# Performance work log

Measured on AMD Instinct MI355X. Metric: run time of the kernel, lower is better.

Reference implementation:

```python
import jax, jax.numpy as jnp
import numpy as np

NTIPS = 128   # taxa
NSITES = 1024 # unique site patterns
BS = 32       # batch of trees


def _make_pairs(ntips, bs, seed=0):
    """Valid postorder child/parent triples for random caterpillar trees.

    Mirrors Parsimony._score's child_parent_pairs: [ntips-1, bs, 3], where the
    last step's torch parent=-1 is rewritten to the last state slot 2*ntips-2.
    """
    rng = np.random.default_rng(seed)
    N = 2 * ntips - 1
    pairs = np.zeros((ntips - 1, bs, 3), dtype=np.int32)
    for b in range(bs):
        leaves = rng.permutation(ntips)
        pairs[0, b] = [leaves[0], leaves[1], ntips]
        for i in range(1, ntips - 3):
            pairs[i, b] = [ntips + i - 1, leaves[i + 1], ntips + i]
        root = 2 * ntips - 3
        pairs[ntips - 3, b] = [2 * ntips - 4, leaves[ntips - 2], root]
        pairs[ntips - 2, b] = [root, leaves[ntips - 1], N - 1]
    return pairs


def setup_inputs() -> dict:
    key = jax.random.key(0)
    k1, k2 = jax.random.split(key)
    # one-hot nucleotide states over 5 symbols (A,G,C,T,-)
    nuc = jax.random.randint(k1, (NTIPS, NSITES), 0, 4)
    L = jax.nn.one_hot(nuc, 5, dtype=jnp.int32).transpose(0, 2, 1)  # [ntips,5,S]
    site_counts = jax.random.randint(k2, (NSITES,), 1, 100).astype(jnp.int32)
    pairs = jnp.asarray(_make_pairs(NTIPS, BS))  # [ntips-1, bs, 3]
    return {"L": L, "site_counts": site_counts, "pairs": pairs}


def reference(L, site_counts, pairs):
    ntips, _, S = L.shape
    steps, bs, _ = pairs.shape
    N = 2 * ntips - 1
    base = jnp.concatenate(
        [L, jnp.zeros((N - ntips, 5, S), dtype=L.dtype)], axis=0)  # [N,5,S]
    state0 = jnp.tile(base[None], (bs, 1, 1, 1))   # [bs,N,5,S]
    score0 = jnp.zeros((bs, S), jnp.int32)
    barange = jnp.arange(bs)

    def step(carry, pair):
        state, score = carry
        child, parent = pair[:, :2], pair[:, 2]            # [bs,2], [bs]
        cs = state[barange[:, None], child]                # gather -> [bs,2,5,S]
        inter = cs[:, 0] * cs[:, 1]                        # [bs,5,S]
        union = ((cs[:, 0] + cs[:, 1]) > 0).astype(L.dtype)
        empty = inter.sum(axis=1, keepdims=True) == 0      # [bs,1,S]
        nxt = jnp.where(empty, union, inter)               # Fitch rule
        state = state.at[barange, parent].set(nxt)         # scatter
        score = score + empty[:, 0].astype(jnp.int32)
        return (state, score), None

    (_, score), _ = jax.lax.scan(step, (state0, score0), pairs)
    return jnp.sum(score * site_counts[None, :], axis=-1)  # [bs]
```

## Files before the change

kernel.cpp:

```cpp
#include <hip/hip_runtime.h>
#include <stdint.h>

#define NTIPS 128
#define NSITES 1024
#define BS 32
#define STEPS 127
#define NINTERNAL 127

__global__ __launch_bounds__(1024) void fitch_kernel(
    const int* __restrict__ L,
    const int* __restrict__ site_counts,
    const int* __restrict__ pairs,
    uint8_t* __restrict__ ws,
    int* __restrict__ out)
{
    __shared__ int spairs[STEPS * 3];
    __shared__ int wsum[16];
    __shared__ int allvalid;

    const int tid  = threadIdx.x;
    const int b    = blockIdx.x;
    const int site = tid;

    if (tid == 0) allvalid = 1;
    if (tid < STEPS * 3) {
        int s = tid / 3, j = tid - s * 3;
        spairs[tid] = pairs[s * (BS * 3) + b * 3 + j];
    }
    __syncthreads();

    if (tid < STEPS) {
        int c0 = spairs[3 * tid], c1 = spairs[3 * tid + 1], p = spairs[3 * tid + 2];
        bool v = (c1 >= 0) && (c1 < NTIPS) && (p >= NTIPS) &&
                 (tid == 0 ? (c0 >= 0 && c0 < NTIPS)
                           : (c0 == spairs[3 * (tid - 1) + 2]));
        if (!v) allvalid = 0;
    }
    __syncthreads();

    const int* Lp = L + site;
    int score = 0;

    #define LEAFMASK(q) ((q)[0] | ((q)[NSITES] << 1) | ((q)[2 * NSITES] << 2) | \
                         ((q)[3 * NSITES] << 3) | ((q)[4 * NSITES] << 4))

    if (allvalid) {
        int c00 = __builtin_amdgcn_readfirstlane(spairs[0]);
        const int* q0 = Lp + c00 * 5 * NSITES;
        int cur = LEAFMASK(q0);
        #pragma unroll 8
        for (int s = 0; s < STEPS; ++s) {
            int c1 = __builtin_amdgcn_readfirstlane(spairs[3 * s + 1]);
            const int* q = Lp + c1 * 5 * NSITES;
            int m1 = LEAFMASK(q);
            int inter = cur & m1;
            score += (inter == 0);
            cur = inter ? inter : (cur | m1);
        }
    } else {
        uint8_t* st = ws + (size_t)b * NINTERNAL * NSITES;
        int lastP = -1, lastV = 0;
        for (int s = 0; s < STEPS; ++s) {
            int c0 = __builtin_amdgcn_readfirstlane(spairs[3 * s]);
            int c1 = __builtin_amdgcn_readfirstlane(spairs[3 * s + 1]);
            int p  = __builtin_amdgcn_readfirstlane(spairs[3 * s + 2]);
            int m0, m1;
            if (c0 == lastP)        m0 = lastV;
            else if (c0 < NTIPS)  { const int* q = Lp + c0 * 5 * NSITES; m0 = LEAFMASK(q); }
            else                    m0 = st[(c0 - NTIPS) * NSITES + site];
            if (c1 == lastP)        m1 = lastV;
            else if (c1 < NTIPS)  { const int* q = Lp + c1 * 5 * NSITES; m1 = LEAFMASK(q); }
            else                    m1 = st[(c1 - NTIPS) * NSITES + site];
            int inter = m0 & m1;
            int nxt   = inter ? inter : (m0 | m1);
            score    += (inter == 0);
            st[(p - NTIPS) * NSITES + site] = (uint8_t)nxt;
            lastP = p; lastV = nxt;
        }
    }

    int val = score * site_counts[site];
    #pragma unroll
    for (int off = 32; off; off >>= 1) val += __shfl_down(val, off);
    if ((tid & 63) == 0) wsum[tid >> 6] = val;
    __syncthreads();
    if (tid == 0) {
        int t = 0;
        #pragma unroll
        for (int i = 0; i < 16; ++i) t += wsum[i];
        out[b] = t;
    }
}

extern "C" void kernel_launch(void* const* d_in, const int* in_sizes, int n_in,
                              void* d_out, int out_size, void* d_ws, size_t ws_size,
                              hipStream_t stream) {
    const int* L           = (const int*)d_in[0];
    const int* site_counts = (const int*)d_in[1];
    const int* pairs       = (const int*)d_in[2];
    fitch_kernel<<<dim3(BS), dim3(1024), 0, stream>>>(
        L, site_counts, pairs, (uint8_t*)d_ws, (int*)d_out);
}
```

Measured before the change: 82.38 us.

## Split each tree across 16 single-wave blocks and combine partial scores atomically

Replaces 32 blocks of 1024 threads with 512 blocks of 64 threads, each handling a 64-site slice of one tree. The goal is to spread work over many more CUs, since 32 blocks leave most of the MI355X idle during the serial 127-step chain. Partial sums are combined with atomicAdd into an output zeroed by a memset. This adds a second launch (the memset) and atomics, and each block now reloads and validates the pair table itself.

```diff
diff --git a/kernel.cpp b/kernel.cpp
--- a/kernel.cpp
+++ b/kernel.cpp
@@ -5,37 +5,50 @@
 #define NSITES 1024
 #define BS 32
 #define STEPS 127
-#define NINTERNAL 127
+#define NNODES 255
+#define SB 64
+#define GPB 16
 
-__global__ __launch_bounds__(1024) void fitch_kernel(
+__global__ __launch_bounds__(64) void fitch_kernel(
     const int* __restrict__ L,
     const int* __restrict__ site_counts,
     const int* __restrict__ pairs,
     uint8_t* __restrict__ ws,
     int* __restrict__ out)
 {
-    __shared__ int spairs[STEPS * 3];
-    __shared__ int wsum[16];
-    __shared__ int allvalid;
+    __shared__ int sc0[STEPS];
+    __shared__ int sc1[STEPS];
+    __shared__ int sp[STEPS];
+    __shared__ int sinvalid;
 
     const int tid  = threadIdx.x;
-    const int b    = blockIdx.x;
-    const int site = tid;
+    const int b    = blockIdx.x >> 4;
+    const int g    = blockIdx.x & (GPB - 1);
+    const int site = (g << 6) + tid;
 
-    if (tid == 0) allvalid = 1;
-    if (tid < STEPS * 3) {
-        int s = tid / 3, j = tid - s * 3;
-        spairs[tid] = pairs[s * (BS * 3) + b * 3 + j];
+    if (tid == 0) sinvalid = 0;
+
+    int c0a[2];
+    bool bad = false;
+    #pragma unroll
+    for (int k = 0; k < 2; ++k) {
+        int i = tid + (k << 6);
+        if (i < STEPS) {
+            const int* pp = pairs + i * (BS * 3) + b * 3;
+            int c0 = pp[0], c1 = pp[1], p = pp[2];
+            sc0[i] = c0; sc1[i] = c1; sp[i] = p;
+            c0a[k] = c0;
+            bad |= ((unsigned)c1 >= NTIPS) || (p < NTIPS) || (p >= NNODES);
+        }
     }
     __syncthreads();
-
-    if (tid < STEPS) {
-        int c0 = spairs[3 * tid], c1 = spairs[3 * tid + 1], p = spairs[3 * tid + 2];
-        bool v = (c1 >= 0) && (c1 < NTIPS) && (p >= NTIPS) &&
-                 (tid == 0 ? (c0 >= 0 && c0 < NTIPS)
-                           : (c0 == spairs[3 * (tid - 1) + 2]));
-        if (!v) allvalid = 0;
+    #pragma unroll
+    for (int k = 0; k < 2; ++k) {
+        int i = tid + (k << 6);
+        if (i < STEPS)
+            bad |= (i == 0) ? ((unsigned)c0a[k] >= NTIPS) : (c0a[k] != sp[i - 1]);
     }
+    if (bad) sinvalid = 1;
     __syncthreads();
 
     const int* Lp = L + site;
@@ -44,13 +57,13 @@
     #define LEAFMASK(q) ((q)[0] | ((q)[NSITES] << 1) | ((q)[2 * NSITES] << 2) | \
                          ((q)[3 * NSITES] << 3) | ((q)[4 * NSITES] << 4))
 
-    if (allvalid) {
-        int c00 = __builtin_amdgcn_readfirstlane(spairs[0]);
+    if (!sinvalid) {
+        int c00 = __builtin_amdgcn_readfirstlane(sc0[0]);
         const int* q0 = Lp + c00 * 5 * NSITES;
         int cur = LEAFMASK(q0);
         #pragma unroll 8
         for (int s = 0; s < STEPS; ++s) {
-            int c1 = __builtin_amdgcn_readfirstlane(spairs[3 * s + 1]);
+            int c1 = __builtin_amdgcn_readfirstlane(sc1[s]);
             const int* q = Lp + c1 * 5 * NSITES;
             int m1 = LEAFMASK(q);
             int inter = cur & m1;
@@ -58,23 +71,23 @@
             cur = inter ? inter : (cur | m1);
         }
     } else {
-        uint8_t* st = ws + (size_t)b * NINTERNAL * NSITES;
+        uint8_t* st = ws + (size_t)blockIdx.x * STEPS * SB;
         int lastP = -1, lastV = 0;
         for (int s = 0; s < STEPS; ++s) {
-            int c0 = __builtin_amdgcn_readfirstlane(spairs[3 * s]);
-            int c1 = __builtin_amdgcn_readfirstlane(spairs[3 * s + 1]);
-            int p  = __builtin_amdgcn_readfirstlane(spairs[3 * s + 2]);
+            int c0 = __builtin_amdgcn_readfirstlane(sc0[s]);
+            int c1 = __builtin_amdgcn_readfirstlane(sc1[s]);
+            int p  = __builtin_amdgcn_readfirstlane(sp[s]);
             int m0, m1;
-            if (c0 == lastP)        m0 = lastV;
-            else if (c0 < NTIPS)  { const int* q = Lp + c0 * 5 * NSITES; m0 = LEAFMASK(q); }
-            else                    m0 = st[(c0 - NTIPS) * NSITES + site];
-            if (c1 == lastP)        m1 = lastV;
-            else if (c1 < NTIPS)  { const int* q = Lp + c1 * 5 * NSITES; m1 = LEAFMASK(q); }
-            else                    m1 = st[(c1 - NTIPS) * NSITES + site];
+            if (c0 == lastP)       m0 = lastV;
+            else if (c0 < NTIPS) { const int* q = Lp + c0 * 5 * NSITES; m0 = LEAFMASK(q); }
+            else                   m0 = st[(c0 - NTIPS) * SB + tid];
+            if (c1 == lastP)       m1 = lastV;
+            else if (c1 < NTIPS) { const int* q = Lp + c1 * 5 * NSITES; m1 = LEAFMASK(q); }
+            else                   m1 = st[(c1 - NTIPS) * SB + tid];
             int inter = m0 & m1;
             int nxt   = inter ? inter : (m0 | m1);
             score    += (inter == 0);
-            st[(p - NTIPS) * NSITES + site] = (uint8_t)nxt;
+            st[(p - NTIPS) * SB + tid] = (uint8_t)nxt;
             lastP = p; lastV = nxt;
         }
     }
@@ -82,14 +95,7 @@
     int val = score * site_counts[site];
     #pragma unroll
     for (int off = 32; off; off >>= 1) val += __shfl_down(val, off);
-    if ((tid & 63) == 0) wsum[tid >> 6] = val;
-    __syncthreads();
-    if (tid == 0) {
-        int t = 0;
-        #pragma unroll
-        for (int i = 0; i < 16; ++i) t += wsum[i];
-        out[b] = t;
-    }
+    if (tid == 0) atomicAdd(&out[b], val);
 }
 
 extern "C" void kernel_launch(void* const* d_in, const int* in_sizes, int n_in,
@@ -98,6 +104,9 @@
     const int* L           = (const int*)d_in[0];
     const int* site_counts = (const int*)d_in[1];
     const int* pairs       = (const int*)d_in[2];
-    fitch_kernel<<<dim3(BS), dim3(1024), 0, stream>>>(
-        L, site_counts, pairs, (uint8_t*)d_ws, (int*)d_out);
+    int* out               = (int*)d_out;
+
+    hipMemsetAsync(out, 0, BS * sizeof(int), stream);
+    fitch_kernel<<<dim3(BS * GPB), dim3(SB), 0, stream>>>(
+        L, site_counts, pairs, (uint8_t*)d_ws, out);
 }
```

Result: faster. 70.70 us (-14.2%).
